# Performance work log

Measured on AMD Instinct MI355X. Metric: run time of the kernel, lower is better.

Reference implementation:

```python
import jax, jax.numpy as jnp
import numpy as np

B, S, E = 2, 2048, 1024
H = 16
HD = E // H           # 64
KD = 64               # k_dim
VD = 64               # v_dim
SCALE = 1.0 / np.float32(np.sqrt(KD))


def setup_inputs() -> dict:
    key = jax.random.key(0)
    ks = jax.random.split(key, 10)
    return {
        "x": jax.random.normal(ks[0], (B, S, E), dtype=jnp.float32),
        "mask": jax.random.uniform(ks[1], (S, S), dtype=jnp.float32),
        "Wq": jax.random.normal(ks[2], (HD, KD), dtype=jnp.float32) * 0.05,
        "bq": jax.random.normal(ks[3], (KD,), dtype=jnp.float32) * 0.05,
        "Wk": jax.random.normal(ks[4], (HD, KD), dtype=jnp.float32) * 0.05,
        "bk": jax.random.normal(ks[5], (KD,), dtype=jnp.float32) * 0.05,
        "Wv": jax.random.normal(ks[6], (HD, VD), dtype=jnp.float32) * 0.05,
        "bv": jax.random.normal(ks[7], (VD,), dtype=jnp.float32) * 0.05,
        "Wo": jax.random.normal(ks[8], (H * VD, E), dtype=jnp.float32) * 0.05,
        "bo": jax.random.normal(ks[9], (E,), dtype=jnp.float32) * 0.05,
    }


def reference(x, mask, Wq, bq, Wk, bk, Wv, bv, Wo, bo):
    b, s, e = x.shape
    # (B, S, E) -> (B, H, S, head_dim)
    xh = x.reshape(b, s, H, HD).transpose(0, 2, 1, 3)
    q = jnp.einsum('bhsd,dk->bhsk', xh, Wq) + bq   # (B,H,S,KD)
    k = jnp.einsum('bhsd,dk->bhsk', xh, Wk) + bk   # (B,H,S,KD)
    v = jnp.einsum('bhsd,dv->bhsv', xh, Wv) + bv   # (B,H,S,VD)
    sim = jnp.einsum('bhqk,bhsk->bhqs', q, k) * SCALE  # (B,H,S,S)
    sim = sim * mask[None, None, :, :]                  # multiplicative mask
    attn = jax.nn.softmax(sim, axis=-1)
    out = jnp.einsum('bhqs,bhsv->bhqv', attn, v)        # (B,H,S,VD)
    out = out.transpose(0, 2, 1, 3).reshape(b, s, H * VD)
    return out @ Wo + bo
```

## Files before the change

kernel.cpp:

```cpp
#include <hip/hip_runtime.h>
#include <hip/hip_bf16.h>

#define SS 2048
#define EE 1024
#define SCALE 0.125f
#define LOG2E 1.44269504088896f

typedef __attribute__((ext_vector_type(8))) short short8;
typedef __attribute__((ext_vector_type(4))) float float4v;
typedef __attribute__((ext_vector_type(4))) unsigned int uint4v;

__device__ __forceinline__ unsigned short f2bf(float f) {
  unsigned int u = __float_as_uint(f);
  unsigned int lsb = (u >> 16) & 1u;
  u += 0x7fffu + lsb;
  return (unsigned short)(u >> 16);
}
__device__ __forceinline__ unsigned int pk2bf(float a, float b) {
  __hip_bfloat162 h = __float22bfloat162_rn(float2{a, b});
  return *reinterpret_cast<unsigned int*>(&h);
}

__global__ __launch_bounds__(256) void prep_kernel(
    const float* __restrict__ mask,
    const float* __restrict__ Wq, const float* __restrict__ Wk,
    const float* __restrict__ Wv,
    unsigned short* __restrict__ maskP, unsigned short* __restrict__ W3T)
{
  __shared__ unsigned short t[64 * 65];
  int blk = blockIdx.x;
  int tid = threadIdx.x;
  if (blk < 2048) {
    int idx = blk * 256 + tid;
    int lane = idx & 63, step = (idx >> 6) & 63, qt = idx >> 12;
    int li = lane & 15, g = lane >> 4;
    const float c = SCALE * LOG2E;
    const float* mrow = mask + (size_t)(qt * 16 + li) * SS + step * 32 + g * 4;
    float4 a = *(const float4*)mrow;
    float4 bb = *(const float4*)(mrow + 16);
    uint4v o;
    o.x = pk2bf(a.x * c, a.y * c);
    o.y = pk2bf(a.z * c, a.w * c);
    o.z = pk2bf(bb.x * c, bb.y * c);
    o.w = pk2bf(bb.z * c, bb.w * c);
    *(uint4v*)(maskP + (size_t)idx * 8) = o;
    return;
  }
  int m = blk - 2048;
  const float* W = (m == 0) ? Wq : (m == 1 ? Wk : Wv);
#pragma unroll
  for (int i = 0; i < 16; ++i) {
    int e = tid + i * 256; int d = e >> 6, n = e & 63;
    t[n * 65 + d] = f2bf(W[e]);
  }
  __syncthreads();
  unsigned short* dst = W3T + m * 4096;
#pragma unroll
  for (int i = 0; i < 16; ++i) {
    int e = tid + i * 256; int n = e >> 6, d = e & 63;
    dst[n * 64 + d] = t[n * 65 + d];
  }
}

__global__ __launch_bounds__(256) void qkv_kernel(
    const float* __restrict__ x, const unsigned short* __restrict__ W3T,
    const float* __restrict__ bq, const float* __restrict__ bk,
    const float* __restrict__ bv,
    unsigned short* __restrict__ Q, unsigned short* __restrict__ Kp,
    unsigned short* __restrict__ Vf)
{
  __shared__ __align__(16) unsigned short w3t[192 * 72];
  __shared__ __align__(16) unsigned short xt[64 * 72];
  __shared__ __align__(16) unsigned short ob[12288];
  __shared__ float sBias[192];
  int tid = threadIdx.x;
  int bh = blockIdx.x >> 4;
  int s0blk = (blockIdx.x & 15) * 128;
  int b = bh >> 4, h = bh & 15;
  int wv = tid >> 6, lane = tid & 63;
  int li = lane & 15, g = lane >> 4;

#pragma unroll
  for (int i = 0; i < 6; ++i) {
    int slot = tid + i * 256;
    int row = slot >> 3, c = slot & 7;
    *(short8*)(w3t + row * 72 + c * 8) = *(const short8*)(W3T + slot * 8);
  }
  if (tid < 192) sBias[tid] = (tid < 64) ? bq[tid] : (tid < 128 ? bk[tid - 64] : bv[tid - 128]);

  for (int half = 0; half < 2; ++half) {
    int s0 = s0blk + half * 64;
    if (half) __syncthreads();
    const float* xbase = x + ((size_t)(b * SS + s0)) * EE + h * 64;
#pragma unroll
    for (int it = 0; it < 4; ++it) {
      int flat = tid + it * 256;
      int row = flat >> 4, ch = flat & 15;
      float4 v = *(const float4*)(xbase + (size_t)row * EE + ch * 4);
      uint2 u; u.x = pk2bf(v.x, v.y); u.y = pk2bf(v.z, v.w);
      *(uint2*)(xt + row * 72 + ch * 4) = u;
    }
    __syncthreads();

    int mrow = wv * 16;
    short8 af[2];
#pragma unroll
    for (int ks = 0; ks < 2; ++ks)
      af[ks] = *(const short8*)(xt + (mrow + li) * 72 + ks * 32 + g * 8);

    float4v acc[12];
#pragma unroll
    for (int i = 0; i < 12; ++i) acc[i] = (float4v){0, 0, 0, 0};
#pragma unroll
    for (int ks = 0; ks < 2; ++ks)
#pragma unroll
      for (int nb = 0; nb < 12; ++nb) {
        short8 bfr = *(const short8*)(w3t + (nb * 16 + li) * 72 + ks * 32 + g * 8);
        acc[nb] = __builtin_amdgcn_mfma_f32_16x16x32_bf16(af[ks], bfr, acc[nb], 0, 0, 0);
      }

#pragma unroll
    for (int nb = 0; nb < 12; ++nb) {
      float bias = sBias[nb * 16 + li];
      int mtx = nb >> 2, sub = nb & 3;
#pragma unroll
      for (int r = 0; r < 4; ++r) {
        unsigned short v = f2bf(acc[nb][r] + bias);
        int sl = mrow + g * 4 + r;
        int stp = sl >> 5, s5 = sl & 31;
        if (mtx == 0) {
          ob[sl * 64 + sub * 16 + li] = v;
        } else if (mtx == 1) {
          int sb = s5 >> 4, lik = s5 & 15;
          int part = sub >> 1;
          int gk = ((sub & 1) << 1) | (li >> 3);
          ob[4096 + stp * 2048 + (sb * 2 + part) * 512 + (gk * 16 + lik) * 8 + (li & 7)] = v;
        } else {
          int pos = ((s5 >> 2) & 3) * 8 + ((s5 >> 4) & 1) * 4 + (s5 & 3);
          ob[8192 + stp * 2048 + sub * 512 + ((pos >> 3) * 16 + li) * 8 + (pos & 7)] = v;
        }
      }
    }
    __syncthreads();

    unsigned short* Qg = Q + ((size_t)bh * SS + s0) * 64;
    unsigned short* Kg = Kp + (size_t)bh * 131072 + (s0 >> 5) * 2048;
    unsigned short* Vg = Vf + (size_t)bh * 131072 + (s0 >> 5) * 2048;
#pragma unroll
    for (int i = 0; i < 6; ++i) {
      int slot = tid + i * 256;
      int rgn = slot >> 9, off = (slot & 511) * 8;
      short8 v = *(const short8*)(ob + rgn * 4096 + off);
      unsigned short* dst = (rgn == 0) ? (Qg + off) : (rgn == 1 ? (Kg + off) : (Vg + off));
      *(short8*)dst = v;
    }
  }
}

__global__ __launch_bounds__(256) void attn_kernel(
    const unsigned short* __restrict__ Q, const unsigned short* __restrict__ Kp,
    const unsigned short* __restrict__ Vf, const unsigned short* __restrict__ maskP,
    unsigned short* __restrict__ AO)
{
  __shared__ __align__(16) unsigned short tr_all[4 * 32 * 72];
  int tid = threadIdx.x, wv = tid >> 6, lane = tid & 63;
  int li = lane & 15, g = lane >> 4;
  int wave_id = blockIdx.x * 4 + wv;
  int bh = wave_id >> 6;
  int q0 = (wave_id & 63) * 32;

  short8 qf[2][2];
#pragma unroll
  for (int t = 0; t < 2; ++t) {
    const unsigned short* Qb = Q + ((size_t)bh * SS + q0 + t * 16 + li) * 64;
    qf[t][0] = *(const short8*)(Qb + g * 8);
    qf[t][1] = *(const short8*)(Qb + 32 + g * 8);
  }

  const unsigned short* Kg = Kp + (size_t)bh * 131072 + lane * 8;
  const unsigned short* Vg = Vf + (size_t)bh * 131072 + lane * 8;
  const unsigned short* Mg0 = maskP + (size_t)(q0 >> 4) * 32768 + lane * 8;
  const unsigned short* Mg1 = Mg0 + 32768;

  unsigned short ov = (li == 0) ? (unsigned short)0x3F80 : (unsigned short)0;
  short8 vones = {(short)ov, (short)ov, (short)ov, (short)ov,
                  (short)ov, (short)ov, (short)ov, (short)ov};

  float4v acc[2][4];
#pragma unroll
  for (int t = 0; t < 2; ++t)
#pragma unroll
    for (int nb = 0; nb < 4; ++nb) acc[t][nb] = (float4v){0, 0, 0, 0};
  float4v accd[2] = {{0, 0, 0, 0}, {0, 0, 0, 0}};

  short8 kf[4];
#pragma unroll
  for (int i = 0; i < 4; ++i) kf[i] = *(const short8*)(Kg + i * 512);
  uint4v mc0 = *(const uint4v*)Mg0;
  uint4v mc1 = *(const uint4v*)Mg1;

  for (int step = 0; step < 64; ++step) {
    int ns = (step + 1) & 63;
    short8 vf[4];
#pragma unroll
    for (int i = 0; i < 4; ++i)
      vf[i] = *(const short8*)(Vg + (size_t)step * 2048 + i * 512);
    short8 kn[4];
#pragma unroll
    for (int i = 0; i < 4; ++i)
      kn[i] = *(const short8*)(Kg + (size_t)ns * 2048 + i * 512);
    uint4v mn0 = *(const uint4v*)(Mg0 + (size_t)ns * 512);
    uint4v mn1 = *(const uint4v*)(Mg1 + (size_t)ns * 512);

    short8 pf[2];
#pragma unroll
    for (int t = 0; t < 2; ++t) {
      uint4v pw;
#pragma unroll
      for (int sb = 0; sb < 2; ++sb) {
        float4v st = {0, 0, 0, 0};
        st = __builtin_amdgcn_mfma_f32_16x16x32_bf16(kf[sb * 2], qf[t][0], st, 0, 0, 0);
        st = __builtin_amdgcn_mfma_f32_16x16x32_bf16(kf[sb * 2 + 1], qf[t][1], st, 0, 0, 0);
#pragma unroll
        for (int hh = 0; hh < 2; ++hh) {
          unsigned int mm = (t == 0) ? mc0[sb * 2 + hh] : mc1[sb * 2 + hh];
          float p0 = __builtin_amdgcn_exp2f(st[2 * hh] * __uint_as_float(mm << 16));
          float p1 = __builtin_amdgcn_exp2f(st[2 * hh + 1] * __uint_as_float(mm & 0xffff0000u));
          pw[sb * 2 + hh] = pk2bf(p0, p1);
        }
      }
      pf[t] = *(short8*)&pw;
    }
#pragma unroll
    for (int nb = 0; nb < 4; ++nb) {
      acc[0][nb] = __builtin_amdgcn_mfma_f32_16x16x32_bf16(vf[nb], pf[0], acc[0][nb], 0, 0, 0);
      acc[1][nb] = __builtin_amdgcn_mfma_f32_16x16x32_bf16(vf[nb], pf[1], acc[1][nb], 0, 0, 0);
    }
    accd[0] = __builtin_amdgcn_mfma_f32_16x16x32_bf16(vones, pf[0], accd[0], 0, 0, 0);
    accd[1] = __builtin_amdgcn_mfma_f32_16x16x32_bf16(vones, pf[1], accd[1], 0, 0, 0);

#pragma unroll
    for (int i = 0; i < 4; ++i) kf[i] = kn[i];
    mc0 = mn0; mc1 = mn1;
  }

  unsigned short* tr = tr_all + wv * (32 * 72);
#pragma unroll
  for (int t = 0; t < 2; ++t) {
    float den = __shfl(accd[t][0], li, 64);
    float rd = 1.0f / den;
#pragma unroll
    for (int nb = 0; nb < 4; ++nb) {
      int base = (t * 16 + li) * 72 + nb * 16 + g * 4;
      *(unsigned int*)(tr + base)     = pk2bf(acc[t][nb][0] * rd, acc[t][nb][1] * rd);
      *(unsigned int*)(tr + base + 2) = pk2bf(acc[t][nb][2] * rd, acc[t][nb][3] * rd);
    }
  }
  asm volatile("s_waitcnt lgkmcnt(0)" ::: "memory");

  int b = bh >> 4, h = bh & 15;
  int rrow = lane >> 3, part = lane & 7;
#pragma unroll
  for (int i = 0; i < 4; ++i) {
    int row = i * 8 + rrow;
    short8 o = *(const short8*)(tr + row * 72 + part * 8);
    *(short8*)(AO + ((size_t)(b * SS + q0 + row)) * EE + h * 64 + part * 8) = o;
  }
}

__global__ __launch_bounds__(256) void out_gemm(
    const unsigned short* __restrict__ AO, const float* __restrict__ Wo,
    const float* __restrict__ bo, float* __restrict__ out)
{
  __shared__ __align__(16) unsigned short at[128 * 72];
  __shared__ __align__(16) unsigned short bt[64 * 72];
  int tid = threadIdx.x, wv = tid >> 6, lane = tid & 63;
  int li = lane & 15, g = lane >> 4;
  int m0 = (blockIdx.x >> 4) * 128;
  int n0 = (blockIdx.x & 15) * 64;
  int wm = (wv & 1) * 64, wn = (wv >> 1) * 32;

  const unsigned short* Ag = AO + (size_t)m0 * 1024;
  const float* Bg = Wo + n0;
  int srow = tid >> 3, scol = (tid & 7) * 8;
  int bkrow = tid >> 4, bch = tid & 15;

  short8 apre[4];
  float4 bpre[4];
  auto ldst = [&](int k0) {
#pragma unroll
    for (int i = 0; i < 4; ++i)
      apre[i] = *(const short8*)(Ag + (size_t)(srow + i * 32) * 1024 + k0 + scol);
#pragma unroll
    for (int i = 0; i < 4; ++i)
      bpre[i] = *(const float4*)(Bg + (size_t)(k0 + bkrow + i * 16) * 1024 + bch * 4);
  };

  float4v acc[4][2];
#pragma unroll
  for (int mt = 0; mt < 4; ++mt)
#pragma unroll
    for (int nt = 0; nt < 2; ++nt) acc[mt][nt] = (float4v){0, 0, 0, 0};

  ldst(0);
  for (int k0 = 0; k0 < 1024; k0 += 64) {
    __syncthreads();
#pragma unroll
    for (int i = 0; i < 4; ++i)
      *(short8*)(at + (srow + i * 32) * 72 + scol) = apre[i];
#pragma unroll
    for (int i = 0; i < 4; ++i) {
      int kr = bkrow + i * 16;
      float4 v = bpre[i];
      bt[(bch * 4 + 0) * 72 + kr] = f2bf(v.x);
      bt[(bch * 4 + 1) * 72 + kr] = f2bf(v.y);
      bt[(bch * 4 + 2) * 72 + kr] = f2bf(v.z);
      bt[(bch * 4 + 3) * 72 + kr] = f2bf(v.w);
    }
    int nk = (k0 + 64 < 1024) ? k0 + 64 : 0;
    ldst(nk);
    __syncthreads();
#pragma unroll
    for (int ks = 0; ks < 2; ++ks) {
      short8 afr[4], bfr[2];
#pragma unroll
      for (int mt = 0; mt < 4; ++mt)
        afr[mt] = *(const short8*)(at + (wm + mt * 16 + li) * 72 + ks * 32 + g * 8);
#pragma unroll
      for (int nt = 0; nt < 2; ++nt)
        bfr[nt] = *(const short8*)(bt + (wn + nt * 16 + li) * 72 + ks * 32 + g * 8);
#pragma unroll
      for (int mt = 0; mt < 4; ++mt)
#pragma unroll
        for (int nt = 0; nt < 2; ++nt)
          acc[mt][nt] = __builtin_amdgcn_mfma_f32_16x16x32_bf16(afr[mt], bfr[nt], acc[mt][nt], 0, 0, 0);
    }
  }
#pragma unroll
  for (int nt = 0; nt < 2; ++nt) {
    float bof = bo[n0 + wn + nt * 16 + li];
#pragma unroll
    for (int mt = 0; mt < 4; ++mt)
#pragma unroll
      for (int r = 0; r < 4; ++r)
        out[(size_t)(m0 + wm + mt * 16 + g * 4 + r) * 1024 + n0 + wn + nt * 16 + li] =
            acc[mt][nt][r] + bof;
  }
}

extern "C" void kernel_launch(void* const* d_in, const int* in_sizes, int n_in,
                              void* d_out, int out_size, void* d_ws, size_t ws_size,
                              hipStream_t stream) {
  const float* x    = (const float*)d_in[0];
  const float* mask = (const float*)d_in[1];
  const float* Wq   = (const float*)d_in[2];
  const float* bq   = (const float*)d_in[3];
  const float* Wk   = (const float*)d_in[4];
  const float* bk   = (const float*)d_in[5];
  const float* Wv   = (const float*)d_in[6];
  const float* bv   = (const float*)d_in[7];
  const float* Wo   = (const float*)d_in[8];
  const float* bo   = (const float*)d_in[9];
  float* out = (float*)d_out;

  unsigned short* ws = (unsigned short*)d_ws;
  unsigned short* Q     = ws;
  unsigned short* Kp    = ws + 4194304;
  unsigned short* Vf    = ws + 8388608;
  unsigned short* AO    = ws + 12582912;
  unsigned short* maskP = ws + 16777216;
  unsigned short* W3T = AO;

  prep_kernel<<<2051, 256, 0, stream>>>(mask, Wq, Wk, Wv, maskP, W3T);
  qkv_kernel<<<512, 256, 0, stream>>>(x, W3T, bq, bk, bv, Q, Kp, Vf);
  attn_kernel<<<512, 256, 0, stream>>>(Q, Kp, Vf, maskP, AO);
  out_gemm<<<512, 256, 0, stream>>>(AO, Wo, bo, out);
}
```

Measured before the change: 189.4 us.

## Double-buffer K, V and mask register prefetch two steps ahead in attention loop

Replaces the single-step K/mask prefetch and in-step V load with two register buffer sets (A/B) and unrolls the loop by two. Each step now issues the loads for the tile two steps ahead, K and mask after the QK/exp phase and V after the PV MFMAs. This gives global loads more time to land before use and removes the V load latency from the critical path. In exchange it raises VGPR pressure, which may lower occupancy or cause spills.

```diff
diff --git a/kernel.cpp b/kernel.cpp
--- a/kernel.cpp
+++ b/kernel.cpp
@@ -193,25 +193,22 @@
     for (int nb = 0; nb < 4; ++nb) acc[t][nb] = (float4v){0, 0, 0, 0};
   float4v accd[2] = {{0, 0, 0, 0}, {0, 0, 0, 0}};
 
-  short8 kf[4];
-#pragma unroll
-  for (int i = 0; i < 4; ++i) kf[i] = *(const short8*)(Kg + i * 512);
-  uint4v mc0 = *(const uint4v*)Mg0;
-  uint4v mc1 = *(const uint4v*)Mg1;
-
-  for (int step = 0; step < 64; ++step) {
-    int ns = (step + 1) & 63;
-    short8 vf[4];
-#pragma unroll
-    for (int i = 0; i < 4; ++i)
-      vf[i] = *(const short8*)(Vg + (size_t)step * 2048 + i * 512);
-    short8 kn[4];
-#pragma unroll
-    for (int i = 0; i < 4; ++i)
-      kn[i] = *(const short8*)(Kg + (size_t)ns * 2048 + i * 512);
-    uint4v mn0 = *(const uint4v*)(Mg0 + (size_t)ns * 512);
-    uint4v mn1 = *(const uint4v*)(Mg1 + (size_t)ns * 512);
-
+  short8 kA[4], kB[4], vA[4], vB[4];
+  uint4v mA0, mA1, mB0, mB1;
+#pragma unroll
+  for (int i = 0; i < 4; ++i) {
+    kA[i] = *(const short8*)(Kg + i * 512);
+    vA[i] = *(const short8*)(Vg + i * 512);
+    kB[i] = *(const short8*)(Kg + 2048 + i * 512);
+    vB[i] = *(const short8*)(Vg + 2048 + i * 512);
+  }
+  mA0 = *(const uint4v*)Mg0;
+  mA1 = *(const uint4v*)Mg1;
+  mB0 = *(const uint4v*)(Mg0 + 512);
+  mB1 = *(const uint4v*)(Mg1 + 512);
+
+  auto do_step = [&](short8 (&kf)[4], short8 (&vf)[4], uint4v& m0c, uint4v& m1c,
+                     int pfs) {
     short8 pf[2];
 #pragma unroll
     for (int t = 0; t < 2; ++t) {
@@ -223,7 +220,7 @@
         st = __builtin_amdgcn_mfma_f32_16x16x32_bf16(kf[sb * 2 + 1], qf[t][1], st, 0, 0, 0);
 #pragma unroll
         for (int hh = 0; hh < 2; ++hh) {
-          unsigned int mm = (t == 0) ? mc0[sb * 2 + hh] : mc1[sb * 2 + hh];
+          unsigned int mm = (t == 0) ? m0c[sb * 2 + hh] : m1c[sb * 2 + hh];
           float p0 = __builtin_amdgcn_exp2f(st[2 * hh] * __uint_as_float(mm << 16));
           float p1 = __builtin_amdgcn_exp2f(st[2 * hh + 1] * __uint_as_float(mm & 0xffff0000u));
           pw[sb * 2 + hh] = pk2bf(p0, p1);
@@ -232,16 +229,25 @@
       pf[t] = *(short8*)&pw;
     }
 #pragma unroll
+    for (int i = 0; i < 4; ++i)
+      kf[i] = *(const short8*)(Kg + (size_t)pfs * 2048 + i * 512);
+    m0c = *(const uint4v*)(Mg0 + (size_t)pfs * 512);
+    m1c = *(const uint4v*)(Mg1 + (size_t)pfs * 512);
+#pragma unroll
     for (int nb = 0; nb < 4; ++nb) {
       acc[0][nb] = __builtin_amdgcn_mfma_f32_16x16x32_bf16(vf[nb], pf[0], acc[0][nb], 0, 0, 0);
       acc[1][nb] = __builtin_amdgcn_mfma_f32_16x16x32_bf16(vf[nb], pf[1], acc[1][nb], 0, 0, 0);
     }
     accd[0] = __builtin_amdgcn_mfma_f32_16x16x32_bf16(vones, pf[0], accd[0], 0, 0, 0);
     accd[1] = __builtin_amdgcn_mfma_f32_16x16x32_bf16(vones, pf[1], accd[1], 0, 0, 0);
-
-#pragma unroll
-    for (int i = 0; i < 4; ++i) kf[i] = kn[i];
-    mc0 = mn0; mc1 = mn1;
+#pragma unroll
+    for (int i = 0; i < 4; ++i)
+      vf[i] = *(const short8*)(Vg + (size_t)pfs * 2048 + i * 512);
+  };
+
+  for (int su = 0; su < 32; ++su) {
+    do_step(kA, vA, mA0, mA1, (2 * su + 2) & 63);
+    do_step(kB, vB, mB0, mB1, (2 * su + 3) & 63);
   }
 
   unsigned short* tr = tr_all + wv * (32 * 72);
```

New measurement: 185.0 us. -2.4%, faster.
